# Kernel optimization log

Hardware: AMD Instinct MI355X
Metric: run time of the kernel (lower is better)

The kernel has to match this reference:

```python
import jax, jax.numpy as jnp
import numpy as np

N_EMBD = 1024
N_HEAD = 16
HEAD = N_EMBD // N_HEAD
D_FF = 4 * N_EMBD
B, T = 2, 2048


def setup_inputs() -> dict:
    key = jax.random.key(0)
    ks = jax.random.split(key, 12)
    s = 0.02
    return {
        "x": jax.random.normal(ks[0], (B, T, N_EMBD), jnp.float32),
        "Wq": jax.random.normal(ks[1], (N_EMBD, N_EMBD), jnp.float32) * s,
        "bq": jnp.zeros((N_EMBD,), jnp.float32),
        "Wk": jax.random.normal(ks[2], (N_EMBD, N_EMBD), jnp.float32) * s,
        "bk": jnp.zeros((N_EMBD,), jnp.float32),
        "Wv": jax.random.normal(ks[3], (N_EMBD, N_EMBD), jnp.float32) * s,
        "bv": jnp.zeros((N_EMBD,), jnp.float32),
        "Wo": jax.random.normal(ks[4], (N_EMBD, N_EMBD), jnp.float32) * s,
        "bo": jnp.zeros((N_EMBD,), jnp.float32),
        "W1": jax.random.normal(ks[5], (N_EMBD, D_FF), jnp.float32) * s,
        "b1": jnp.zeros((D_FF,), jnp.float32),
        "W2": jax.random.normal(ks[6], (D_FF, N_EMBD), jnp.float32) * s,
        "b2": jnp.zeros((N_EMBD,), jnp.float32),
        "g1": jnp.ones((N_EMBD,), jnp.float32),
        "be1": jnp.zeros((N_EMBD,), jnp.float32),
        "g2": jnp.ones((N_EMBD,), jnp.float32),
        "be2": jnp.zeros((N_EMBD,), jnp.float32),
    }


def _layernorm(x, g, b, eps=1e-3):
    # keras LayerNormalization default epsilon=1e-3
    mu = jnp.mean(x, axis=-1, keepdims=True)
    var = jnp.mean(jnp.square(x - mu), axis=-1, keepdims=True)
    return (x - mu) * jax.lax.rsqrt(var + eps) * g + b


def _attention(h, Wq, bq, Wk, bk, Wv, bv, Wo, bo):
    b, t, _ = h.shape
    q = (h @ Wq + bq).reshape(b, t, N_HEAD, HEAD)
    k = (h @ Wk + bk).reshape(b, t, N_HEAD, HEAD)
    v = (h @ Wv + bv).reshape(b, t, N_HEAD, HEAD)
    scores = jnp.einsum("bthd,bshd->bhts", q, k) / jnp.sqrt(jnp.float32(HEAD))
    causal = jnp.tril(jnp.ones((t, t), bool))
    scores = jnp.where(causal, scores, -jnp.inf)
    w = jax.nn.softmax(scores, axis=-1)  # dropout is identity in eval
    ctx = jnp.einsum("bhts,bshd->bthd", w, v).reshape(b, t, N_EMBD)
    return ctx @ Wo + bo


def reference(x, Wq, bq, Wk, bk, Wv, bv, Wo, bo, W1, b1, W2, b2, g1, be1, g2, be2):
    x = x + _attention(_layernorm(x, g1, be1), Wq, bq, Wk, bk, Wv, bv, Wo, bo)
    h = _layernorm(x, g2, be2)
    ff = jax.nn.relu(h @ W1 + b1) @ W2 + b2
    return x + ff
```

## Files before the change

### kernel.cpp

```cpp
#include <hip/hip_runtime.h>

typedef __bf16 bf16;
typedef __attribute__((ext_vector_type(8))) __bf16 bf16x8;
typedef __attribute__((ext_vector_type(4))) __bf16 bf16x4;
typedef __attribute__((ext_vector_type(4))) float f32x4;

#define MFMA16(A, B, C) __builtin_amdgcn_mfma_f32_16x16x32_bf16(A, B, C, 0, 0, 0)

#define GLOAD16(gp, lp)                                          \
  __builtin_amdgcn_global_load_lds(                              \
      (const __attribute__((address_space(1))) void*)(gp),       \
      (__attribute__((address_space(3))) void*)(lp), 16, 0, 0)

__device__ __forceinline__ float fexp2(float x) {
#if __has_builtin(__builtin_amdgcn_exp2f)
  return __builtin_amdgcn_exp2f(x);
#else
  float r;
  asm("v_exp_f32 %0, %1" : "=v"(r) : "v"(x));
  return r;
#endif
}

#define QSCL 0.18033688011112042f

__global__ __launch_bounds__(256) void prologue_kernel(
    const float* __restrict__ w0, const float* __restrict__ w1,
    const float* __restrict__ w2, const float* __restrict__ w3,
    bf16* __restrict__ out4,
    const float* __restrict__ W1, bf16* __restrict__ w1t,
    const float* __restrict__ W2, bf16* __restrict__ w2t,
    const float* __restrict__ x, const float* __restrict__ gamma,
    const float* __restrict__ beta, bf16* __restrict__ h1)
{
  __shared__ float tile[32][33];
  __shared__ float ssum[4], ssq[4];
  const int bid = blockIdx.x;

  if (bid >= 12288) {
    const int row = bid - 12288;
    const int t = threadIdx.y * 32 + threadIdx.x;
    const float4 v = ((const float4*)(x + (size_t)row * 1024))[t];
    float s = v.x + v.y + v.z + v.w;
    float sq = v.x * v.x + v.y * v.y + v.z * v.z + v.w * v.w;
#pragma unroll
    for (int m = 1; m < 64; m <<= 1) {
      s += __shfl_xor(s, m);
      sq += __shfl_xor(sq, m);
    }
    const int wv = t >> 6;
    if ((t & 63) == 0) { ssum[wv] = s; ssq[wv] = sq; }
    __syncthreads();
    s = ssum[0] + ssum[1] + ssum[2] + ssum[3];
    sq = ssq[0] + ssq[1] + ssq[2] + ssq[3];
    const float mu = s * (1.0f / 1024.0f);
    const float var = sq * (1.0f / 1024.0f) - mu * mu;
    const float rs = rsqrtf(var + 1e-3f);
    const float4 g = ((const float4*)gamma)[t];
    const float4 b = ((const float4*)beta)[t];
    bf16x4 o;
    o[0] = (bf16)((v.x - mu) * rs * g.x + b.x);
    o[1] = (bf16)((v.y - mu) * rs * g.y + b.y);
    o[2] = (bf16)((v.z - mu) * rs * g.z + b.z);
    o[3] = (bf16)((v.w - mu) * rs * g.w + b.w);
    *(bf16x4*)(h1 + (size_t)row * 1024 + t * 4) = o;
    return;
  }

  const float* in;
  bf16* out;
  int K, N, kt, nt;
  if (bid < 4096) {
    const float* srcs[4] = {w0, w1, w2, w3};
    in = srcs[bid >> 10];
    out = out4 + (size_t)(bid >> 10) * 1024 * 1024;
    K = 1024; N = 1024;
    const int t = bid & 1023;
    nt = (t & 31) * 32; kt = (t >> 5) * 32;
  } else if (bid < 8192) {
    in = W1; out = w1t; K = 1024; N = 4096;
    const int t = bid - 4096;
    nt = (t & 127) * 32; kt = (t >> 7) * 32;
  } else {
    in = W2; out = w2t; K = 4096; N = 1024;
    const int t = bid - 8192;
    nt = (t & 31) * 32; kt = (t >> 5) * 32;
  }
  const int tx = threadIdx.x, ty = threadIdx.y;
#pragma unroll
  for (int j = 0; j < 4; ++j)
    tile[ty + j * 8][tx] = in[(size_t)(kt + ty + j * 8) * N + nt + tx];
  __syncthreads();
#pragma unroll
  for (int j = 0; j < 4; ++j)
    out[(size_t)(nt + ty + j * 8) * K + kt + tx] = (bf16)tile[tx][ty + j * 8];
}

__global__ __launch_bounds__(256) void ln_b_kernel(
    const bf16* __restrict__ in, const float* __restrict__ gamma,
    const float* __restrict__ beta, bf16* __restrict__ out)
{
  const int row = blockIdx.x;
  const int t = threadIdx.x;
  const bf16x4 vb = *(const bf16x4*)(in + (size_t)row * 1024 + t * 4);
  float v0 = (float)vb[0], v1 = (float)vb[1], v2 = (float)vb[2], v3 = (float)vb[3];
  float s = v0 + v1 + v2 + v3;
  float sq = v0 * v0 + v1 * v1 + v2 * v2 + v3 * v3;
#pragma unroll
  for (int m = 1; m < 64; m <<= 1) {
    s += __shfl_xor(s, m);
    sq += __shfl_xor(sq, m);
  }
  __shared__ float ssum[4], ssq[4];
  const int w = t >> 6;
  if ((t & 63) == 0) { ssum[w] = s; ssq[w] = sq; }
  __syncthreads();
  s = ssum[0] + ssum[1] + ssum[2] + ssum[3];
  sq = ssq[0] + ssq[1] + ssq[2] + ssq[3];
  const float mu = s * (1.0f / 1024.0f);
  const float var = sq * (1.0f / 1024.0f) - mu * mu;
  const float rs = rsqrtf(var + 1e-3f);
  const float4 g = ((const float4*)gamma)[t];
  const float4 b = ((const float4*)beta)[t];
  bf16x4 o;
  o[0] = (bf16)((v0 - mu) * rs * g.x + b.x);
  o[1] = (bf16)((v1 - mu) * rs * g.y + b.y);
  o[2] = (bf16)((v2 - mu) * rs * g.z + b.z);
  o[3] = (bf16)((v3 - mu) * rs * g.w + b.w);
  *(bf16x4*)(out + (size_t)row * 1024 + t * 4) = o;
}

template <int BM, int BN, int BK, int EPI, int SWZ>
__global__ __launch_bounds__(256, 2) void gemm_bt(
    const bf16* __restrict__ A, const bf16* __restrict__ Bt,
    const float* __restrict__ bias0, const float* __restrict__ bias1,
    const float* __restrict__ bias2, const float* __restrict__ resid,
    const bf16* __restrict__ residb,
    bf16* __restrict__ out0, bf16* __restrict__ out1, bf16* __restrict__ out2,
    float* __restrict__ outf, int M, int N, int K)
{
  constexpr int WM = BM / 2, WN = BN / 2;
  constexpr int MI = WM / 16, NJ = WN / 16;
  constexpr int KK = BK / 32;
  constexpr int NSLOT = BK / 8;
  constexpr int SMASK = NSLOT - 1;
  constexpr int RPL = 512 / BK;
  constexpr int ALOADS = BM / (4 * RPL);
  constexpr int BLOADS = BN / (4 * RPL);
  constexpr int S = ALOADS + BLOADS;

  __shared__ bf16 As[3][BM * BK];
  __shared__ bf16 Bs[3][BN * BK];
  const int tid = threadIdx.x;
  const int lane = tid & 63, w = tid >> 6;
  const int wr = w >> 1, wc = w & 1;
  const int g = lane >> 4, lr = lane & 15;

  int bx = blockIdx.x, by = blockIdx.y;
  if constexpr (SWZ) {
    const int bid = bx + gridDim.x * by;
    const int xcd = bid & 7, idx = bid >> 3;
    const int chunk = gridDim.y >> 3;
    by = xcd * chunk + (idx % chunk);
    bx = idx / chunk;
  }
  const int brow = by * BM, bcol = bx * BN;

  f32x4 acc[MI][NJ] = {};

  const int lrow = lane / NSLOT;
  const int slot = lane & SMASK;
  int lcol;
  if constexpr (BK == 32)
    lcol = ((slot - (lrow >> 1)) & 3) * 8;
  else
    lcol = (slot ^ (lrow & 7)) * 8;

  auto stage = [&](int buf, int k0) {
#pragma unroll
    for (int j = 0; j < ALOADS; ++j) {
      const int row0 = w * (BM / 4) + j * RPL;
      GLOAD16(A + (size_t)(brow + row0 + lrow) * K + k0 + lcol,
              &As[buf][row0 * BK]);
    }
#pragma unroll
    for (int j = 0; j < BLOADS; ++j) {
      const int row0 = w * (BN / 4) + j * RPL;
      GLOAD16(Bt + (size_t)(bcol + row0 + lrow) * K + k0 + lcol,
              &Bs[buf][row0 * BK]);
    }
  };

  auto rdslot = [&](int kg) {
    if constexpr (BK == 32) return ((kg + (lr >> 1)) & 3) * 8;
    else return (kg ^ (lr & 7)) * 8;
  };

  const int nk = K / BK;
  stage(0, 0);
  stage(1, BK);
  int cur = 0;
  for (int t = 0; t < nk; ++t) {
    if (t + 1 < nk) {
      if constexpr (S == 3)
        asm volatile("s_waitcnt vmcnt(3)" ::: "memory");
      else if constexpr (S == 4)
        asm volatile("s_waitcnt vmcnt(4)" ::: "memory");
      else
        asm volatile("s_waitcnt vmcnt(6)" ::: "memory");
    } else {
      asm volatile("s_waitcnt vmcnt(0)" ::: "memory");
    }
    __builtin_amdgcn_s_barrier();
    __builtin_amdgcn_sched_barrier(0);

    bf16x8 afr[MI][KK], bfr[NJ][KK];
#pragma unroll
    for (int i = 0; i < MI; ++i)
#pragma unroll
      for (int kk = 0; kk < KK; ++kk)
        afr[i][kk] = *(const bf16x8*)&As[cur][(wr * WM + i * 16 + lr) * BK +
                                             rdslot(kk * 4 + g)];
#pragma unroll
    for (int j = 0; j < NJ; ++j)
#pragma unroll
      for (int kk = 0; kk < KK; ++kk)
        bfr[j][kk] = *(const bf16x8*)&Bs[cur][(wc * WN + j * 16 + lr) * BK +
                                             rdslot(kk * 4 + g)];

    if (t + 2 < nk) {
      int nb = cur + 2;
      if (nb >= 3) nb -= 3;
      stage(nb, (t + 2) * BK);
    }

    __builtin_amdgcn_s_setprio(1);
#pragma unroll
    for (int kk = 0; kk < KK; ++kk)
#pragma unroll
      for (int i = 0; i < MI; ++i)
#pragma unroll
        for (int j = 0; j < NJ; ++j)
          acc[i][j] = MFMA16(afr[i][kk], bfr[j][kk], acc[i][j]);
    __builtin_amdgcn_s_setprio(0);

    ++cur;
    if (cur == 3) cur = 0;
  }

#pragma unroll
  for (int i = 0; i < MI; ++i) {
#pragma unroll
    for (int j = 0; j < NJ; ++j) {
      const int r0 = brow + wr * WM + i * 16 + g * 4;
      const int c = bcol + wc * WN + j * 16 + lr;
      if constexpr (EPI == 1) {
        const float bv = bias0[c];
#pragma unroll
        for (int rr = 0; rr < 4; ++rr)
          out0[(size_t)(r0 + rr) * N + c] =
              (bf16)fmaxf(acc[i][j][rr] + bv, 0.0f);
      } else if constexpr (EPI == 5) {
        const float bv = bias0[c];
#pragma unroll
        for (int rr = 0; rr < 4; ++rr) {
          const size_t idx = (size_t)(r0 + rr) * N + c;
          out0[idx] = (bf16)(acc[i][j][rr] + bv + resid[idx]);
        }
      } else if constexpr (EPI == 6) {
        const float bv = bias0[c];
#pragma unroll
        for (int rr = 0; rr < 4; ++rr) {
          const size_t idx = (size_t)(r0 + rr) * N + c;
          outf[idx] = acc[i][j][rr] + bv + (float)residb[idx];
        }
      } else {
        const int sub = c >> 10;
        const int c1 = c & 1023;
        if (sub == 0) {
          const float bv = bias0[c1];
#pragma unroll
          for (int rr = 0; rr < 4; ++rr)
            out0[(size_t)(r0 + rr) * 1024 + c1] =
                (bf16)((acc[i][j][rr] + bv) * QSCL);
        } else if (sub == 1) {
          const float bv = bias1[c1];
#pragma unroll
          for (int rr = 0; rr < 4; ++rr)
            out1[(size_t)(r0 + rr) * 1024 + c1] = (bf16)(acc[i][j][rr] + bv);
        } else {
          const float bv = bias2[c1];
          const int bb = r0 >> 11, t0 = r0 & 2047;
          const int hh = c1 >> 6, dd = c1 & 63;
          bf16x4 pk;
#pragma unroll
          for (int rr = 0; rr < 4; ++rr) pk[rr] = (bf16)(acc[i][j][rr] + bv);
          *(bf16x4*)(out2 + ((size_t)((bb * 16 + hh) * 64 + dd)) * 2048 + t0) = pk;
        }
      }
    }
  }
}

__global__ __launch_bounds__(256) void attn_kernel(
    const bf16* __restrict__ q, const bf16* __restrict__ kmat,
    const bf16* __restrict__ vt, bf16* __restrict__ ctx)
{
  __shared__ bf16 Ks[64 * 64];
  __shared__ bf16 Vs[64 * 64];
  __shared__ bf16 Pq[4][16][72];
  const int bx = blockIdx.x, by = blockIdx.y;
  const int k4 = by >> 3;
  const int qt = (k4 == 0) ? bx
               : (k4 == 1) ? (31 - bx)
               : (k4 == 2) ? (bx ^ 16)
                           : (31 - (bx ^ 16));
  const int b_ = by >> 4, h_ = by & 15;
  const int qb = qt * 64;
  const int tid = threadIdx.x;
  const int lane = tid & 63, w = tid >> 6;
  const int g = lane >> 4, lr = lane & 15;
  const int qrow = qb + w * 16 + lr;

  bf16x8 qf[2];
  {
    const bf16* qp = q + (size_t)(b_ * 2048 + qrow) * 1024 + h_ * 64 + g * 8;
    qf[0] = *(const bf16x8*)qp;
    qf[1] = *(const bf16x8*)(qp + 32);
  }

  f32x4 o[4] = {};
  float l = 0.f;

  const int srow = tid >> 2;
  const int c16 = (tid & 3) * 16;
  const int rb = srow * 128;
  const int sw = (srow & 7) << 4;
  const bf16* kbase = kmat + (size_t)(b_ * 2048) * 1024 + h_ * 64;
  const bf16* vbase = vt + (size_t)(b_ * 16 + h_) * 64 * 2048;
  const bf16* kp0 = kbase + (size_t)srow * 1024 + c16;
  const bf16* vp0 = vbase + (size_t)srow * 2048 + c16;

  bf16x8 k0 = *(const bf16x8*)kp0;
  bf16x8 k1 = *(const bf16x8*)(kp0 + 8);
  bf16x8 v0 = *(const bf16x8*)vp0;
  bf16x8 v1 = *(const bf16x8*)(vp0 + 8);

  for (int s0 = 0; s0 <= qb; s0 += 64) {
    *(bf16x8*)((char*)Ks + ((rb + c16 * 2) ^ sw)) = k0;
    *(bf16x8*)((char*)Ks + ((rb + c16 * 2 + 16) ^ sw)) = k1;
    *(bf16x8*)((char*)Vs + ((rb + c16 * 2) ^ sw)) = v0;
    *(bf16x8*)((char*)Vs + ((rb + c16 * 2 + 16) ^ sw)) = v1;
    __syncthreads();
    if (s0 < qb) {
      const bf16* kp = kp0 + (size_t)(s0 + 64) * 1024;
      k0 = *(const bf16x8*)kp;
      k1 = *(const bf16x8*)(kp + 8);
      const bf16* vp = vp0 + (s0 + 64);
      v0 = *(const bf16x8*)vp;
      v1 = *(const bf16x8*)(vp + 8);
    }

    f32x4 st[4];
    __builtin_amdgcn_s_setprio(1);
#pragma unroll
    for (int n = 0; n < 4; ++n) {
      f32x4 z = {};
#pragma unroll
      for (int kk = 0; kk < 2; ++kk) {
        const int row = n * 16 + lr;
        bf16x8 ak = *(const bf16x8*)((char*)Ks +
            ((row * 128 + kk * 64 + g * 16) ^ ((lr & 7) << 4)));
        z = MFMA16(ak, qf[kk], z);
      }
      st[n] = z;
    }
    __builtin_amdgcn_s_setprio(0);

    if (s0 == qb) {
#pragma unroll
      for (int n = 0; n < 4; ++n)
#pragma unroll
        for (int r = 0; r < 4; ++r)
          if (s0 + n * 16 + g * 4 + r > qrow) st[n][r] = -1e30f;
    }

    float rs = 0.f;
#pragma unroll
    for (int n = 0; n < 4; ++n) {
      bf16x4 pk;
#pragma unroll
      for (int r = 0; r < 4; ++r) {
        const float p = fexp2(st[n][r]);
        rs += p;
        pk[r] = (bf16)p;
      }
      *(bf16x4*)&Pq[w][lr][n * 16 + g * 4] = pk;
    }

    bf16x8 pa[2];
#pragma unroll
    for (int kk = 0; kk < 2; ++kk)
      pa[kk] = *(const bf16x8*)&Pq[w][lr][kk * 32 + g * 8];
    __builtin_amdgcn_s_setprio(1);
#pragma unroll
    for (int n = 0; n < 4; ++n) {
      const int row = n * 16 + lr;
#pragma unroll
      for (int kk = 0; kk < 2; ++kk) {
        bf16x8 bv = *(const bf16x8*)((char*)Vs +
            ((row * 128 + kk * 64 + g * 16) ^ ((lr & 7) << 4)));
        o[n] = MFMA16(pa[kk], bv, o[n]);
      }
    }
    __builtin_amdgcn_s_setprio(0);

    rs += __shfl_xor(rs, 16);
    rs += __shfl_xor(rs, 32);
    l += rs;
    __syncthreads();
  }

  float lq[4];
#pragma unroll
  for (int r = 0; r < 4; ++r) lq[r] = __shfl(l, g * 4 + r);
#pragma unroll
  for (int r = 0; r < 4; ++r) {
    const float inv = 1.0f / lq[r];
#pragma unroll
    for (int n = 0; n < 4; ++n)
      ctx[(size_t)(b_ * 2048 + qb + w * 16 + g * 4 + r) * 1024 + h_ * 64 + n * 16 + lr] =
          (bf16)(o[n][r] * inv);
  }
}

extern "C" void kernel_launch(void* const* d_in, const int* in_sizes, int n_in,
                              void* d_out, int out_size, void* d_ws, size_t ws_size,
                              hipStream_t stream)
{
  (void)in_sizes; (void)n_in; (void)out_size; (void)ws_size;
  const float* x   = (const float*)d_in[0];
  const float* Wq  = (const float*)d_in[1];
  const float* bq  = (const float*)d_in[2];
  const float* Wk  = (const float*)d_in[3];
  const float* bk  = (const float*)d_in[4];
  const float* Wv  = (const float*)d_in[5];
  const float* bv  = (const float*)d_in[6];
  const float* Wo  = (const float*)d_in[7];
  const float* bo  = (const float*)d_in[8];
  const float* W1  = (const float*)d_in[9];
  const float* b1  = (const float*)d_in[10];
  const float* W2  = (const float*)d_in[11];
  const float* b2  = (const float*)d_in[12];
  const float* g1  = (const float*)d_in[13];
  const float* be1 = (const float*)d_in[14];
  const float* g2  = (const float*)d_in[15];
  const float* be2 = (const float*)d_in[16];
  float* out = (float*)d_out;

  char* ws = (char*)d_ws;
  const size_t MB = 1024 * 1024;
  bf16* wqkv_t = (bf16*)(ws + 0 * MB);
  bf16* wo_t = (bf16*)(ws + 6 * MB);
  bf16* w1_t = (bf16*)(ws + 8 * MB);
  bf16* w2_t = (bf16*)(ws + 16 * MB);
  bf16* h1   = (bf16*)(ws + 24 * MB);
  bf16* qbuf = (bf16*)(ws + 32 * MB);
  bf16* kbuf = (bf16*)(ws + 40 * MB);
  bf16* vtb  = (bf16*)(ws + 48 * MB);
  bf16* ctx  = (bf16*)(ws + 56 * MB);
  bf16* h2   = (bf16*)(ws + 64 * MB);
  bf16* x2b  = (bf16*)(ws + 72 * MB);
  bf16* ff1  = (bf16*)(ws + 24 * MB);

  prologue_kernel<<<16384, dim3(32, 8), 0, stream>>>(
      Wq, Wk, Wv, Wo, wqkv_t, W1, w1_t, W2, w2_t, x, g1, be1, h1);

  gemm_bt<128, 128, 32, 4, 1><<<dim3(24, 32), 256, 0, stream>>>(
      h1, wqkv_t, bq, bk, bv, nullptr, nullptr, qbuf, kbuf, vtb, nullptr,
      4096, 3072, 1024);

  attn_kernel<<<dim3(32, 32), 256, 0, stream>>>(qbuf, kbuf, vtb, ctx);

  gemm_bt<128, 64, 64, 5, 0><<<dim3(16, 32), 256, 0, stream>>>(
      ctx, wo_t, bo, nullptr, nullptr, x, nullptr, x2b, nullptr, nullptr,
      nullptr, 4096, 1024, 1024);

  ln_b_kernel<<<4096, 256, 0, stream>>>(x2b, g2, be2, h2);

  gemm_bt<256, 128, 32, 1, 1><<<dim3(32, 16), 256, 0, stream>>>(
      h2, w1_t, b1, nullptr, nullptr, nullptr, nullptr, ff1, nullptr, nullptr,
      nullptr, 4096, 4096, 1024);

  gemm_bt<128, 64, 64, 6, 1><<<dim3(16, 32), 256, 0, stream>>>(
      ff1, w2_t, b2, nullptr, nullptr, nullptr, x2b, nullptr, nullptr, nullptr,
      out, 4096, 1024, 4096);
}
```

Baseline: 195.1 us.

## Share K/V tiles across two adjacent query tiles per 512-thread attention block

The attention kernel now uses 512-thread blocks, with two groups of four waves each handling one of two adjacent 64-row query tiles. Each K/V tile staged in LDS is reused by both query tiles, which halves global K/V traffic and block count. Each thread now loads one 16-byte chunk instead of two. The cost is that the lower query tile's waves sit idle on the last diagonal tile while still joining the barriers, and causal load balancing changes to a simple mirrored pairing.

```diff
diff --git a/kernel.cpp b/kernel.cpp
--- a/kernel.cpp
+++ b/kernel.cpp
@@ -302,25 +302,24 @@
   }
 }
 
-__global__ __launch_bounds__(256) void attn_kernel(
+__global__ __launch_bounds__(512) void attn_kernel(
     const bf16* __restrict__ q, const bf16* __restrict__ kmat,
     const bf16* __restrict__ vt, bf16* __restrict__ ctx)
 {
   __shared__ bf16 Ks[64 * 64];
   __shared__ bf16 Vs[64 * 64];
-  __shared__ bf16 Pq[4][16][72];
+  __shared__ bf16 Pq[8][16][72];
   const int bx = blockIdx.x, by = blockIdx.y;
-  const int k4 = by >> 3;
-  const int qt = (k4 == 0) ? bx
-               : (k4 == 1) ? (31 - bx)
-               : (k4 == 2) ? (bx ^ 16)
-                           : (31 - (bx ^ 16));
+  const int k2 = by >> 4;
+  const int a = k2 ? (15 - bx) : bx;
   const int b_ = by >> 4, h_ = by & 15;
-  const int qb = qt * 64;
   const int tid = threadIdx.x;
   const int lane = tid & 63, w = tid >> 6;
+  const int wg = w >> 2, ww = w & 3;
   const int g = lane >> 4, lr = lane & 15;
-  const int qrow = qb + w * 16 + lr;
+  const int qt = 2 * a + wg;
+  const int qb = qt * 64;
+  const int qrow = qb + ww * 16 + lr;
 
   bf16x8 qf[2];
   {
@@ -332,92 +331,88 @@
   f32x4 o[4] = {};
   float l = 0.f;
 
-  const int srow = tid >> 2;
-  const int c16 = (tid & 3) * 16;
+  const int srow = tid >> 3;
+  const int c8 = (tid & 7) * 8;
   const int rb = srow * 128;
   const int sw = (srow & 7) << 4;
   const bf16* kbase = kmat + (size_t)(b_ * 2048) * 1024 + h_ * 64;
   const bf16* vbase = vt + (size_t)(b_ * 16 + h_) * 64 * 2048;
-  const bf16* kp0 = kbase + (size_t)srow * 1024 + c16;
-  const bf16* vp0 = vbase + (size_t)srow * 2048 + c16;
+  const bf16* kp0 = kbase + (size_t)srow * 1024 + c8;
+  const bf16* vp0 = vbase + (size_t)srow * 2048 + c8;
 
   bf16x8 k0 = *(const bf16x8*)kp0;
-  bf16x8 k1 = *(const bf16x8*)(kp0 + 8);
   bf16x8 v0 = *(const bf16x8*)vp0;
-  bf16x8 v1 = *(const bf16x8*)(vp0 + 8);
-
-  for (int s0 = 0; s0 <= qb; s0 += 64) {
-    *(bf16x8*)((char*)Ks + ((rb + c16 * 2) ^ sw)) = k0;
-    *(bf16x8*)((char*)Ks + ((rb + c16 * 2 + 16) ^ sw)) = k1;
-    *(bf16x8*)((char*)Vs + ((rb + c16 * 2) ^ sw)) = v0;
-    *(bf16x8*)((char*)Vs + ((rb + c16 * 2 + 16) ^ sw)) = v1;
+
+  const int ns = 2 * a + 2;
+  for (int t = 0; t < ns; ++t) {
+    const int s0 = t << 6;
+    *(bf16x8*)((char*)Ks + ((rb + c8 * 2) ^ sw)) = k0;
+    *(bf16x8*)((char*)Vs + ((rb + c8 * 2) ^ sw)) = v0;
     __syncthreads();
-    if (s0 < qb) {
-      const bf16* kp = kp0 + (size_t)(s0 + 64) * 1024;
-      k0 = *(const bf16x8*)kp;
-      k1 = *(const bf16x8*)(kp + 8);
-      const bf16* vp = vp0 + (s0 + 64);
-      v0 = *(const bf16x8*)vp;
-      v1 = *(const bf16x8*)(vp + 8);
-    }
-
-    f32x4 st[4];
-    __builtin_amdgcn_s_setprio(1);
-#pragma unroll
-    for (int n = 0; n < 4; ++n) {
-      f32x4 z = {};
-#pragma unroll
-      for (int kk = 0; kk < 2; ++kk) {
+    if (t + 1 < ns) {
+      k0 = *(const bf16x8*)(kp0 + (size_t)(s0 + 64) * 1024);
+      v0 = *(const bf16x8*)(vp0 + (s0 + 64));
+    }
+
+    if (s0 <= qb) {
+      f32x4 st[4];
+      __builtin_amdgcn_s_setprio(1);
+#pragma unroll
+      for (int n = 0; n < 4; ++n) {
+        f32x4 z = {};
+#pragma unroll
+        for (int kk = 0; kk < 2; ++kk) {
+          const int row = n * 16 + lr;
+          bf16x8 ak = *(const bf16x8*)((char*)Ks +
+              ((row * 128 + kk * 64 + g * 16) ^ ((lr & 7) << 4)));
+          z = MFMA16(ak, qf[kk], z);
+        }
+        st[n] = z;
+      }
+      __builtin_amdgcn_s_setprio(0);
+
+      if (s0 == qb) {
+#pragma unroll
+        for (int n = 0; n < 4; ++n)
+#pragma unroll
+          for (int r = 0; r < 4; ++r)
+            if (s0 + n * 16 + g * 4 + r > qrow) st[n][r] = -1e30f;
+      }
+
+      float rs = 0.f;
+#pragma unroll
+      for (int n = 0; n < 4; ++n) {
+        bf16x4 pk;
+#pragma unroll
+        for (int r = 0; r < 4; ++r) {
+          const float p = fexp2(st[n][r]);
+          rs += p;
+          pk[r] = (bf16)p;
+        }
+        *(bf16x4*)&Pq[w][lr][n * 16 + g * 4] = pk;
+      }
+
+      bf16x8 pa[2];
+#pragma unroll
+      for (int kk = 0; kk < 2; ++kk)
+        pa[kk] = *(const bf16x8*)&Pq[w][lr][kk * 32 + g * 8];
+      __builtin_amdgcn_s_setprio(1);
+#pragma unroll
+      for (int n = 0; n < 4; ++n) {
         const int row = n * 16 + lr;
-        bf16x8 ak = *(const bf16x8*)((char*)Ks +
-            ((row * 128 + kk * 64 + g * 16) ^ ((lr & 7) << 4)));
-        z = MFMA16(ak, qf[kk], z);
+#pragma unroll
+        for (int kk = 0; kk < 2; ++kk) {
+          bf16x8 bv = *(const bf16x8*)((char*)Vs +
+              ((row * 128 + kk * 64 + g * 16) ^ ((lr & 7) << 4)));
+          o[n] = MFMA16(pa[kk], bv, o[n]);
+        }
       }
-      st[n] = z;
-    }
-    __builtin_amdgcn_s_setprio(0);
-
-    if (s0 == qb) {
-#pragma unroll
-      for (int n = 0; n < 4; ++n)
-#pragma unroll
-        for (int r = 0; r < 4; ++r)
-          if (s0 + n * 16 + g * 4 + r > qrow) st[n][r] = -1e30f;
-    }
-
-    float rs = 0.f;
-#pragma unroll
-    for (int n = 0; n < 4; ++n) {
-      bf16x4 pk;
-#pragma unroll
-      for (int r = 0; r < 4; ++r) {
-        const float p = fexp2(st[n][r]);
-        rs += p;
-        pk[r] = (bf16)p;
-      }
-      *(bf16x4*)&Pq[w][lr][n * 16 + g * 4] = pk;
-    }
-
-    bf16x8 pa[2];
-#pragma unroll
-    for (int kk = 0; kk < 2; ++kk)
-      pa[kk] = *(const bf16x8*)&Pq[w][lr][kk * 32 + g * 8];
-    __builtin_amdgcn_s_setprio(1);
-#pragma unroll
-    for (int n = 0; n < 4; ++n) {
-      const int row = n * 16 + lr;
-#pragma unroll
-      for (int kk = 0; kk < 2; ++kk) {
-        bf16x8 bv = *(const bf16x8*)((char*)Vs +
-            ((row * 128 + kk * 64 + g * 16) ^ ((lr & 7) << 4)));
-        o[n] = MFMA16(pa[kk], bv, o[n]);
-      }
-    }
-    __builtin_amdgcn_s_setprio(0);
-
-    rs += __shfl_xor(rs, 16);
-    rs += __shfl_xor(rs, 32);
-    l += rs;
+      __builtin_amdgcn_s_setprio(0);
+
+      rs += __shfl_xor(rs, 16);
+      rs += __shfl_xor(rs, 32);
+      l += rs;
+    }
     __syncthreads();
   }
 
@@ -429,8 +424,8 @@
     const float inv = 1.0f / lq[r];
 #pragma unroll
     for (int n = 0; n < 4; ++n)
-      ctx[(size_t)(b_ * 2048 + qb + w * 16 + g * 4 + r) * 1024 + h_ * 64 + n * 16 + lr] =
-          (bf16)(o[n][r] * inv);
+      ctx[(size_t)(b_ * 2048 + qb + ww * 16 + g * 4 + r) * 1024 + h_ * 64 +
+          n * 16 + lr] = (bf16)(o[n][r] * inv);
   }
 }
 
@@ -480,7 +475,7 @@
       h1, wqkv_t, bq, bk, bv, nullptr, nullptr, qbuf, kbuf, vtb, nullptr,
       4096, 3072, 1024);
 
-  attn_kernel<<<dim3(32, 32), 256, 0, stream>>>(qbuf, kbuf, vtb, ctx);
+  attn_kernel<<<dim3(16, 32), 512, 0, stream>>>(qbuf, kbuf, vtb, ctx);
 
   gemm_bt<128, 64, 64, 5, 0><<<dim3(16, 32), 256, 0, stream>>>(
       ctx, wo_t, bo, nullptr, nullptr, x, nullptr, x2b, nullptr, nullptr,
```

Result: faster. 188.5 us, median of 2 (-3.4%).
